# Kernel tuning notes

Measured on AMD Instinct MI355X. Metric: run time of the kernel, lower is better.

Reference implementation:

```python
import jax, jax.numpy as jnp
import numpy as np

STRIDE = 1
PADDING = 1
DILATION = 1


def setup_inputs() -> dict:
    key = jax.random.key(0)
    k1, k2 = jax.random.split(key)
    x = jax.random.normal(k1, (32, 256, 56, 56), dtype=jnp.float32)
    # weight (C_out, C_in, kh, kw); the torch module reformats this to CSR but
    # the computed convolution is mathematically identical to a dense conv.
    W = jax.random.normal(k2, (256, 256, 3, 3), dtype=jnp.float32) * 0.05
    return {"x": x, "W": W}


def reference(x, W):
    # Faithful to SparseConv2D.forward in Inference_Sparse mode: a standard
    # 2D convolution (groups=1, no bias) with stride/padding/dilation.
    out = jax.lax.conv_general_dilated(
        x, W,
        window_strides=(STRIDE, STRIDE),
        padding=[(PADDING, PADDING), (PADDING, PADDING)],
        rhs_dilation=(DILATION, DILATION),
        dimension_numbers=("NCHW", "OIHW", "NCHW"),
    )
    return out
```

## Files before the change

### kernel.cpp

```cpp
#include <hip/hip_runtime.h>

typedef __bf16 bf16_t;
typedef __attribute__((ext_vector_type(8))) __bf16 bf16x8;
typedef __attribute__((ext_vector_type(4))) float f32x4;

#define IMG_H 56
#define IMG_W 56
#define CIN 256
#define COUT 256
#define TH 8
#define TW 16
#define XR 10
#define XCOL 18
#define CK 32
#define PH 58
#define PW 58
#define NPIX (XR * XCOL)
#define NUNIT (NPIX * 5)
#define NISSUE ((NUNIT + 63) / 64)
#define XS_ELEMS (NPIX * 40)

#define NBLK 1792
#define CPX  (NBLK / 8)

#define XBF_BYTES ((size_t)32 * PH * PW * CIN * 2)
#define WT_BYTES  ((size_t)9 * COUT * CIN * 2)

__global__ void wt_permute(const float* __restrict__ W, bf16_t* __restrict__ wt2) {
    int u = blockIdx.x * 256 + threadIdx.x;
    int lane = u & 63;
    int fn   = (u >> 6) & 7;
    int half = (u >> 9) & 1;
    int ch   = (u >> 10) & 7;
    int t    = u >> 13;
    int g = lane >> 4, pc = lane & 15;
    int k  = half * 128 + fn * 16 + pc;
    int cb = ch * 32 + g * 8;
    bf16x8 v;
    #pragma unroll
    for (int j = 0; j < 8; ++j)
        v[j] = (bf16_t)W[(k * CIN + cb + j) * 9 + t];
    *(bf16x8*)(wt2 + (size_t)u * 8) = v;
}

#define LSP 258
__global__ __launch_bounds__(256)
void x_to_bf16(const float* __restrict__ x, bf16_t* __restrict__ xbf) {
    __shared__ bf16_t ls[IMG_W * LSP];
    const int n = blockIdx.y, ph = blockIdx.x;
    bf16_t* drow = xbf + (size_t)(n * PH + ph) * PW * CIN;
    const f32x4 zf = {0.f, 0.f, 0.f, 0.f};
    if (ph == 0 || ph == PH - 1) {
        for (int i = threadIdx.x; i < PW * CIN / 8; i += 256)
            ((f32x4*)drow)[i] = zf;
        return;
    }
    for (int i = threadIdx.x; i < 2 * CIN / 8; i += 256) {
        int side = i >> 5, off = i & 31;
        ((f32x4*)(drow + (side ? (size_t)(PW - 1) * CIN : 0)))[off] = zf;
    }
    const int h = ph - 1;
    const float* src = x + ((size_t)n * CIN * IMG_H + h) * IMG_W;
    for (int e = threadIdx.x; e < CIN * IMG_W; e += 256) {
        int c = e / IMG_W, w = e - c * IMG_W;
        ls[w * LSP + c] = (bf16_t)src[(size_t)c * (IMG_H * IMG_W) + w];
    }
    __syncthreads();
    bf16_t* dst = drow + CIN;
    for (int i = threadIdx.x; i < IMG_W * (CIN / 8); i += 256) {
        int w = i >> 5, cp = (i & 31) * 8;
        bf16x8 v;
        #pragma unroll
        for (int j = 0; j < 8; ++j) v[j] = ls[w * LSP + cp + j];
        *(bf16x8*)(dst + (size_t)w * CIN + cp) = v;
    }
}

__global__ __launch_bounds__(256, 3)
void conv_mfma(const bf16_t* __restrict__ xbf, const bf16_t* __restrict__ wt2,
               float* __restrict__ out) {
    __shared__ __align__(16) bf16_t xs[2][XS_ELEMS];

    const int tid  = threadIdx.x;
    const int lane = tid & 63;
    const int wid  = tid >> 6;

    const int hw      = blockIdx.x;
    const int logical = (hw & 7) * CPX + (hw >> 3);
    const int bk = logical & 1;
    int tmp = logical >> 1;
    const int wx = tmp & 3;  tmp >>= 2;
    const int hy = tmp % 7;
    const int n  = tmp / 7;
    const int h0 = hy * TH;
    const int w0 = wx * TW;

    const int wm   = wid >> 1;
    const int kq2  = wid & 1;
    const int pc   = lane & 15;
    const int g    = lane >> 4;

    f32x4 acc[4][4] = {};
    const bf16_t* wfrag = wt2 + (size_t)lane * 8 + (size_t)bk * 4096
                              + (size_t)kq2 * 2048;
    const bf16_t* xn = xbf + (size_t)n * (PH * PW * CIN);

    int soff[4];
    #pragma unroll
    for (int s = 0; s < 4; ++s) {
        int j = wid + s * 4;
        int u = j * 64 + lane;
        int p = u / 5, q = u - p * 5;
        bool ok = (j < NISSUE) && (u < NUNIT) && (q < 4);
        int r = p / XCOL, col = p - r * XCOL;
        int w = w0 + col; if (w > PW - 1) w = PW - 1;
        int rr = (r > XR - 1) ? (XR - 1) : r;
        soff[s] = ok ? (((h0 + rr) * PW + w) * CIN + q * 8) : -1;
    }

    auto STAGE = [&](int buf, int ch) {
        #pragma unroll
        for (int s = 0; s < 4; ++s)
            if (soff[s] >= 0)
                __builtin_amdgcn_global_load_lds(
                    (const __attribute__((address_space(1))) void*)(xn + soff[s] + ch * CK),
                    (__attribute__((address_space(3))) void*)(&xs[buf][(wid + s * 4) * 512]),
                    16, 0, 0);
    };

    bf16x8 bcur[4], bnext[4];
    #pragma unroll
    for (int q = 0; q < 4; ++q)
        bcur[q] = *(const bf16x8*)(wfrag + q * 512);
    STAGE(0, 0);
    __syncthreads();

    for (int ch = 0; ch < 8; ++ch) {
        const int cur = ch & 1;
        const bf16_t* wch = wfrag + (size_t)ch * 8192;

        #pragma unroll
        for (int dw = 0; dw < 3; ++dw) {
            bf16x8 a[6];
            #pragma unroll
            for (int r = 0; r < 6; ++r)
                a[r] = *(const bf16x8*)&xs[cur][((wm * 4 + r) * XCOL + pc + dw) * 40 + g * 8];
            #pragma unroll
            for (int dh = 0; dh < 3; ++dh) {
                const bool lastTap = (dw == 2) && (dh == 2);
                const bool doPf = !(lastTap && ch == 7);
                if (doPf) {
                    const int tn = (dh < 2) ? ((dh + 1) * 3 + dw) : (dw + 1);
                    const bf16_t* wp = lastTap ? (wch + 8192)
                                               : (wch + (size_t)tn * 65536);
                    #pragma unroll
                    for (int q = 0; q < 4; ++q)
                        bnext[q] = *(const bf16x8*)(wp + q * 512);
                }
                if (dw == 0 && dh == 1 && ch < 7)
                    STAGE(cur ^ 1, ch + 1);
                __builtin_amdgcn_s_setprio(1);
                #pragma unroll
                for (int fm = 0; fm < 4; ++fm)
                    #pragma unroll
                    for (int q = 0; q < 4; ++q)
                        acc[fm][q] = __builtin_amdgcn_mfma_f32_16x16x32_bf16(
                            a[fm + dh], bcur[q], acc[fm][q], 0, 0, 0);
                __builtin_amdgcn_s_setprio(0);
                if (doPf) {
                    #pragma unroll
                    for (int q = 0; q < 4; ++q) bcur[q] = bnext[q];
                }
            }
        }
        __syncthreads();
    }

    const int wcol = w0 + g * 4;
    if (wcol < IMG_W) {
        #pragma unroll
        for (int fm = 0; fm < 4; ++fm) {
            int hh = h0 + wm * 4 + fm;
            #pragma unroll
            for (int q = 0; q < 4; ++q) {
                int k = bk * 128 + kq2 * 64 + q * 16 + pc;
                *(f32x4*)&out[((n * COUT + k) * IMG_H + hh) * IMG_W + wcol] = acc[fm][q];
            }
        }
    }
}

#define CPAD 40
__global__ __launch_bounds__(256, 2)
void conv_mfma_v2(const float* __restrict__ x, const bf16_t* __restrict__ wt2,
                  float* __restrict__ out) {
    __shared__ bf16_t xsl[XR * XCOL * CPAD];
    const int tid  = threadIdx.x;
    const int lane = tid & 63;
    const int wid  = tid >> 6;
    const int n    = blockIdx.z;
    const int h0   = blockIdx.y * TH;
    const int w0   = blockIdx.x * TW;
    const int wm   = wid >> 1;
    const int half = wid & 1;
    const int pc = lane & 15;
    const int g  = lane >> 4;
    const int c0 = g * 8;
    f32x4 acc[4][8] = {};
    const bf16_t* wch_base = wt2 + (size_t)lane * 8 + (size_t)half * 4096;
    for (int ch = 0; ch < 8; ++ch) {
        __syncthreads();
        for (int e = tid; e < XR * XCOL * CK; e += 256) {
            int col = e % XCOL;
            int r   = (e / XCOL) % XR;
            int ci  = e / (XCOL * XR);
            int hh = h0 - 1 + r;
            int ww = w0 - 1 + col;
            float v = 0.f;
            if ((unsigned)hh < (unsigned)IMG_H && (unsigned)ww < (unsigned)IMG_W)
                v = x[((n * CIN + ch * CK + ci) * IMG_H + hh) * IMG_W + ww];
            xsl[(r * XCOL + col) * CPAD + ci] = (bf16_t)v;
        }
        __syncthreads();
        const bf16_t* wch = wch_base + (size_t)ch * 8192;
        #pragma unroll 3
        for (int t = 0; t < 9; ++t) {
            const int dh = t / 3, dw = t % 3;
            const bf16_t* wp = wch + (size_t)t * 65536;
            bf16x8 b[8];
            #pragma unroll
            for (int fn = 0; fn < 8; ++fn)
                b[fn] = *(const bf16x8*)(wp + fn * 512);
            bf16x8 a[4];
            #pragma unroll
            for (int fm = 0; fm < 4; ++fm)
                a[fm] = *(const bf16x8*)&xsl[((wm * 4 + fm + dh) * XCOL + (pc + dw)) * CPAD + c0];
            #pragma unroll
            for (int fm = 0; fm < 4; ++fm)
                #pragma unroll
                for (int fn = 0; fn < 8; ++fn)
                    acc[fm][fn] = __builtin_amdgcn_mfma_f32_16x16x32_bf16(
                        a[fm], b[fn], acc[fm][fn], 0, 0, 0);
        }
    }
    const int wcol = w0 + g * 4;
    if (wcol < IMG_W) {
        #pragma unroll
        for (int fm = 0; fm < 4; ++fm) {
            int hh = h0 + wm * 4 + fm;
            #pragma unroll
            for (int fn = 0; fn < 8; ++fn) {
                int k = half * 128 + fn * 16 + pc;
                *(f32x4*)&out[((n * COUT + k) * IMG_H + hh) * IMG_W + wcol] = acc[fm][fn];
            }
        }
    }
}

__global__ void conv_naive(const float* __restrict__ x, const float* __restrict__ W,
                           float* __restrict__ out, int total) {
    int i = blockIdx.x * 256 + threadIdx.x;
    if (i >= total) return;
    int w = i % IMG_W;
    int h = (i / IMG_W) % IMG_H;
    int k = (i / (IMG_W * IMG_H)) % COUT;
    int n = i / (IMG_W * IMG_H * COUT);
    float s = 0.f;
    for (int c = 0; c < CIN; ++c) {
        #pragma unroll
        for (int dh = 0; dh < 3; ++dh) {
            int hh = h + dh - 1;
            if ((unsigned)hh >= (unsigned)IMG_H) continue;
            #pragma unroll
            for (int dw = 0; dw < 3; ++dw) {
                int ww = w + dw - 1;
                if ((unsigned)ww >= (unsigned)IMG_W) continue;
                s += x[((n * CIN + c) * IMG_H + hh) * IMG_W + ww] *
                     W[((k * CIN + c) * 3 + dh) * 3 + dw];
            }
        }
    }
    out[i] = s;
}

extern "C" void kernel_launch(void* const* d_in, const int* in_sizes, int n_in,
                              void* d_out, int out_size, void* d_ws, size_t ws_size,
                              hipStream_t stream) {
    const float* x = (const float*)d_in[0];
    const float* W = (const float*)d_in[1];
    float* out = (float*)d_out;

    if (ws_size >= XBF_BYTES + WT_BYTES) {
        bf16_t* xbf = (bf16_t*)d_ws;
        bf16_t* wt2 = (bf16_t*)((char*)d_ws + XBF_BYTES);
        wt_permute<<<dim3(288), dim3(256), 0, stream>>>(W, wt2);
        x_to_bf16<<<dim3(PH, 32), dim3(256), 0, stream>>>(x, xbf);
        conv_mfma<<<dim3(NBLK), dim3(256), 0, stream>>>(xbf, wt2, out);
    } else if (ws_size >= WT_BYTES) {
        bf16_t* wt2 = (bf16_t*)d_ws;
        wt_permute<<<dim3(288), dim3(256), 0, stream>>>(W, wt2);
        conv_mfma_v2<<<dim3(4, 7, 32), dim3(256), 0, stream>>>(x, wt2, out);
    } else {
        int total = 32 * COUT * IMG_H * IMG_W;
        conv_naive<<<dim3((total + 255) / 256), dim3(256), 0, stream>>>(x, W, out, total);
    }
}
```

Baseline: 144.7 us.

## Switch main conv kernel from 16x16x32 to 32x32x16 bf16 MFMA tiles

Replaces the 16x16x32 MFMA inner loop with 32x32x16 MFMAs, each covering two output rows by 16 columns against 32 output channels. The weight permutation gets a matching fragment layout, the LDS A-fragment loads are re-indexed, and the epilogue is rewritten for the 32x32 accumulator layout. The old permutation is kept for the fallback v2 kernel. The aim is fewer MFMA issues and fewer register operand reads per FLOP. It changes the LDS read pattern and register pressure, which may cause bank conflicts.

Result: slower. 176.7 us (+22.2%).

```diff
diff --git a/kernel.cpp b/kernel.cpp
--- a/kernel.cpp
+++ b/kernel.cpp
@@ -3,6 +3,7 @@
 typedef __bf16 bf16_t;
 typedef __attribute__((ext_vector_type(8))) __bf16 bf16x8;
 typedef __attribute__((ext_vector_type(4))) float f32x4;
+typedef __attribute__((ext_vector_type(16))) float f32x16;
 
 #define IMG_H 56
 #define IMG_W 56
@@ -29,6 +30,25 @@
 __global__ void wt_permute(const float* __restrict__ W, bf16_t* __restrict__ wt2) {
     int u = blockIdx.x * 256 + threadIdx.x;
     int lane = u & 63;
+    int frag = u >> 6;
+    int ks   = frag & 1;
+    int nf   = (frag >> 1) & 1;
+    int kq2  = (frag >> 2) & 1;
+    int bk   = (frag >> 3) & 1;
+    int ch   = (frag >> 4) & 7;
+    int t    = frag >> 7;
+    int k  = bk * 128 + kq2 * 64 + nf * 32 + (lane & 31);
+    int cb = ch * 32 + ks * 16 + (lane >> 5) * 8;
+    bf16x8 v;
+    #pragma unroll
+    for (int j = 0; j < 8; ++j)
+        v[j] = (bf16_t)W[(k * CIN + cb + j) * 9 + t];
+    *(bf16x8*)(wt2 + (size_t)u * 8) = v;
+}
+
+__global__ void wt_permute16(const float* __restrict__ W, bf16_t* __restrict__ wt2) {
+    int u = blockIdx.x * 256 + threadIdx.x;
+    int lane = u & 63;
     int fn   = (u >> 6) & 7;
     int half = (u >> 9) & 1;
     int ch   = (u >> 10) & 7;
@@ -95,12 +115,13 @@
     const int h0 = hy * TH;
     const int w0 = wx * TW;
 
-    const int wm   = wid >> 1;
-    const int kq2  = wid & 1;
-    const int pc   = lane & 15;
-    const int g    = lane >> 4;
-
-    f32x4 acc[4][4] = {};
+    const int wm    = wid >> 1;
+    const int kq2   = wid & 1;
+    const int pc    = lane & 15;
+    const int prow  = (lane >> 4) & 1;
+    const int chalf = lane >> 5;
+
+    f32x16 acc32[2][2] = {};
     const bf16_t* wfrag = wt2 + (size_t)lane * 8 + (size_t)bk * 4096
                               + (size_t)kq2 * 2048;
     const bf16_t* xn = xbf + (size_t)n * (PH * PW * CIN);
@@ -141,10 +162,14 @@
 
         #pragma unroll
         for (int dw = 0; dw < 3; ++dw) {
-            bf16x8 a[6];
-            #pragma unroll
-            for (int r = 0; r < 6; ++r)
-                a[r] = *(const bf16x8*)&xs[cur][((wm * 4 + r) * XCOL + pc + dw) * 40 + g * 8];
+            bf16x8 a32[5][2];
+            #pragma unroll
+            for (int re = 0; re < 5; ++re)
+                #pragma unroll
+                for (int ks = 0; ks < 2; ++ks)
+                    a32[re][ks] = *(const bf16x8*)&xs[cur][
+                        ((wm * 4 + re + prow) * XCOL + pc + dw) * 40
+                        + ks * 16 + chalf * 8];
             #pragma unroll
             for (int dh = 0; dh < 3; ++dh) {
                 const bool lastTap = (dw == 2) && (dh == 2);
@@ -161,11 +186,14 @@
                     STAGE(cur ^ 1, ch + 1);
                 __builtin_amdgcn_s_setprio(1);
                 #pragma unroll
-                for (int fm = 0; fm < 4; ++fm)
+                for (int ks = 0; ks < 2; ++ks)
                     #pragma unroll
-                    for (int q = 0; q < 4; ++q)
-                        acc[fm][q] = __builtin_amdgcn_mfma_f32_16x16x32_bf16(
-                            a[fm + dh], bcur[q], acc[fm][q], 0, 0, 0);
+                    for (int mf = 0; mf < 2; ++mf)
+                        #pragma unroll
+                        for (int nf = 0; nf < 2; ++nf)
+                            acc32[mf][nf] = __builtin_amdgcn_mfma_f32_32x32x16_bf16(
+                                a32[mf * 2 + dh][ks], bcur[nf * 2 + ks],
+                                acc32[mf][nf], 0, 0, 0);
                 __builtin_amdgcn_s_setprio(0);
                 if (doPf) {
                     #pragma unroll
@@ -176,15 +204,23 @@
         __syncthreads();
     }
 
-    const int wcol = w0 + g * 4;
-    if (wcol < IMG_W) {
-        #pragma unroll
-        for (int fm = 0; fm < 4; ++fm) {
-            int hh = h0 + wm * 4 + fm;
-            #pragma unroll
-            for (int q = 0; q < 4; ++q) {
-                int k = bk * 128 + kq2 * 64 + q * 16 + pc;
-                *(f32x4*)&out[((n * COUT + k) * IMG_H + hh) * IMG_W + wcol] = acc[fm][q];
+    #pragma unroll
+    for (int mf = 0; mf < 2; ++mf) {
+        #pragma unroll
+        for (int nf = 0; nf < 2; ++nf) {
+            const int k = bk * 128 + kq2 * 64 + nf * 32 + (lane & 31);
+            #pragma unroll
+            for (int r4 = 0; r4 < 4; ++r4) {
+                const int hh   = h0 + wm * 4 + mf * 2 + (r4 >> 1);
+                const int wcol = w0 + (r4 & 1) * 8 + 4 * chalf;
+                if (wcol < IMG_W) {
+                    f32x4 v;
+                    v[0] = acc32[mf][nf][r4 * 4 + 0];
+                    v[1] = acc32[mf][nf][r4 * 4 + 1];
+                    v[2] = acc32[mf][nf][r4 * 4 + 2];
+                    v[3] = acc32[mf][nf][r4 * 4 + 3];
+                    *(f32x4*)&out[((n * COUT + k) * IMG_H + hh) * IMG_W + wcol] = v;
+                }
             }
         }
     }
@@ -298,7 +334,7 @@
         conv_mfma<<<dim3(NBLK), dim3(256), 0, stream>>>(xbf, wt2, out);
     } else if (ws_size >= WT_BYTES) {
         bf16_t* wt2 = (bf16_t*)d_ws;
-        wt_permute<<<dim3(288), dim3(256), 0, stream>>>(W, wt2);
+        wt_permute16<<<dim3(288), dim3(256), 0, stream>>>(W, wt2);
         conv_mfma_v2<<<dim3(4, 7, 32), dim3(256), 0, stream>>>(x, wt2, out);
     } else {
         int total = 32 * COUT * IMG_H * IMG_W;
```

## Retile conv_mfma to 8x8 spatial tiles with all 256 output channels per block

Applied to the files above, without the earlier changes.

The main MFMA kernel's spatial tile changes from 8x16 (plus a K-half split across blocks) to 8x8 with each block computing all 256 output channels, four waves each owning 64 channels. The A-fragment mapping now packs two image rows of 8 columns into each 16-row MFMA tile, and the padded-width waste from 56/16 tiling goes away. This removes the duplicate input staging that came from splitting K across two blocks, so each input halo is loaded once per block. In exchange there are fewer blocks (1568), smaller halos with a larger halo-to-interior ratio, more A registers per wave, and a more complex LDS read pattern that may cause bank conflicts.

After: 155.2 us. 1.07x slower.

```diff
diff --git a/kernel.cpp b/kernel.cpp
--- a/kernel.cpp
+++ b/kernel.cpp
@@ -9,18 +9,18 @@
 #define CIN 256
 #define COUT 256
 #define TH 8
-#define TW 16
+#define TW 8
 #define XR 10
-#define XCOL 18
+#define XCOL 10
 #define CK 32
 #define PH 58
 #define PW 58
 #define NPIX (XR * XCOL)
 #define NUNIT (NPIX * 5)
-#define NISSUE ((NUNIT + 63) / 64)
-#define XS_ELEMS (NPIX * 40)
-
-#define NBLK 1792
+#define NISSUE 8
+#define XS_ELEMS 4096
+
+#define NBLK 1568
 #define CPX  (NBLK / 8)
 
 #define XBF_BYTES ((size_t)32 * PH * PW * CIN * 2)
@@ -87,40 +87,37 @@
 
     const int hw      = blockIdx.x;
     const int logical = (hw & 7) * CPX + (hw >> 3);
-    const int bk = logical & 1;
-    int tmp = logical >> 1;
-    const int wx = tmp & 3;  tmp >>= 2;
-    const int hy = tmp % 7;
-    const int n  = tmp / 7;
-    const int h0 = hy * TH;
-    const int w0 = wx * TW;
-
-    const int wm   = wid >> 1;
-    const int kq2  = wid & 1;
+    const int n   = logical / 49;
+    const int rem = logical - n * 49;
+    const int hy  = rem / 7;
+    const int wx  = rem - hy * 7;
+    const int h0  = hy * TH;
+    const int w0  = wx * TW;
+
     const int pc   = lane & 15;
     const int g    = lane >> 4;
+    const int arow = pc >> 3;
+    const int awc  = pc & 7;
 
     f32x4 acc[4][4] = {};
-    const bf16_t* wfrag = wt2 + (size_t)lane * 8 + (size_t)bk * 4096
-                              + (size_t)kq2 * 2048;
+    const bf16_t* wfrag = wt2 + (size_t)lane * 8 + (size_t)(wid >> 1) * 4096
+                              + (size_t)(wid & 1) * 2048;
     const bf16_t* xn = xbf + (size_t)n * (PH * PW * CIN);
 
-    int soff[4];
+    int soff[2];
     #pragma unroll
-    for (int s = 0; s < 4; ++s) {
+    for (int s = 0; s < 2; ++s) {
         int j = wid + s * 4;
         int u = j * 64 + lane;
         int p = u / 5, q = u - p * 5;
-        bool ok = (j < NISSUE) && (u < NUNIT) && (q < 4);
+        bool ok = (u < NUNIT) && (q < 4);
         int r = p / XCOL, col = p - r * XCOL;
-        int w = w0 + col; if (w > PW - 1) w = PW - 1;
-        int rr = (r > XR - 1) ? (XR - 1) : r;
-        soff[s] = ok ? (((h0 + rr) * PW + w) * CIN + q * 8) : -1;
+        soff[s] = ok ? (((h0 + r) * PW + (w0 + col)) * CIN + q * 8) : -1;
     }
 
     auto STAGE = [&](int buf, int ch) {
         #pragma unroll
-        for (int s = 0; s < 4; ++s)
+        for (int s = 0; s < 2; ++s)
             if (soff[s] >= 0)
                 __builtin_amdgcn_global_load_lds(
                     (const __attribute__((address_space(1))) void*)(xn + soff[s] + ch * CK),
@@ -141,10 +138,11 @@
 
         #pragma unroll
         for (int dw = 0; dw < 3; ++dw) {
-            bf16x8 a[6];
-            #pragma unroll
-            for (int r = 0; r < 6; ++r)
-                a[r] = *(const bf16x8*)&xs[cur][((wm * 4 + r) * XCOL + pc + dw) * 40 + g * 8];
+            bf16x8 a[9];
+            #pragma unroll
+            for (int j = 0; j < 9; ++j)
+                a[j] = *(const bf16x8*)&xs[cur][
+                    ((arow + j) * XCOL + awc + dw) * 40 + g * 8];
             #pragma unroll
             for (int dh = 0; dh < 3; ++dh) {
                 const bool lastTap = (dw == 2) && (dh == 2);
@@ -165,7 +163,7 @@
                     #pragma unroll
                     for (int q = 0; q < 4; ++q)
                         acc[fm][q] = __builtin_amdgcn_mfma_f32_16x16x32_bf16(
-                            a[fm + dh], bcur[q], acc[fm][q], 0, 0, 0);
+                            a[fm * 2 + dh], bcur[q], acc[fm][q], 0, 0, 0);
                 __builtin_amdgcn_s_setprio(0);
                 if (doPf) {
                     #pragma unroll
@@ -176,31 +174,32 @@
         __syncthreads();
     }
 
-    const int wcol = w0 + g * 4;
-    if (wcol < IMG_W) {
-        #pragma unroll
-        for (int fm = 0; fm < 4; ++fm) {
-            int hh = h0 + wm * 4 + fm;
-            #pragma unroll
-            for (int q = 0; q < 4; ++q) {
-                int k = bk * 128 + kq2 * 64 + q * 16 + pc;
-                *(f32x4*)&out[((n * COUT + k) * IMG_H + hh) * IMG_W + wcol] = acc[fm][q];
-            }
-        }
-    }
-}
-
+    const int hhb  = h0 + (g >> 1);
+    const int wcol = w0 + (g & 1) * 4;
+    #pragma unroll
+    for (int fm = 0; fm < 4; ++fm) {
+        const int hh = hhb + fm * 2;
+        #pragma unroll
+        for (int q = 0; q < 4; ++q) {
+            const int k = wid * 64 + q * 16 + pc;
+            *(f32x4*)&out[((n * COUT + k) * IMG_H + hh) * IMG_W + wcol] = acc[fm][q];
+        }
+    }
+}
+
+#define FXR 10
+#define FXCOL 18
 #define CPAD 40
 __global__ __launch_bounds__(256, 2)
 void conv_mfma_v2(const float* __restrict__ x, const bf16_t* __restrict__ wt2,
                   float* __restrict__ out) {
-    __shared__ bf16_t xsl[XR * XCOL * CPAD];
+    __shared__ bf16_t xsl[FXR * FXCOL * CPAD];
     const int tid  = threadIdx.x;
     const int lane = tid & 63;
     const int wid  = tid >> 6;
     const int n    = blockIdx.z;
-    const int h0   = blockIdx.y * TH;
-    const int w0   = blockIdx.x * TW;
+    const int h0   = blockIdx.y * 8;
+    const int w0   = blockIdx.x * 16;
     const int wm   = wid >> 1;
     const int half = wid & 1;
     const int pc = lane & 15;
@@ -210,16 +209,16 @@
     const bf16_t* wch_base = wt2 + (size_t)lane * 8 + (size_t)half * 4096;
     for (int ch = 0; ch < 8; ++ch) {
         __syncthreads();
-        for (int e = tid; e < XR * XCOL * CK; e += 256) {
-            int col = e % XCOL;
-            int r   = (e / XCOL) % XR;
-            int ci  = e / (XCOL * XR);
+        for (int e = tid; e < FXR * FXCOL * CK; e += 256) {
+            int col = e % FXCOL;
+            int r   = (e / FXCOL) % FXR;
+            int ci  = e / (FXCOL * FXR);
             int hh = h0 - 1 + r;
             int ww = w0 - 1 + col;
             float v = 0.f;
             if ((unsigned)hh < (unsigned)IMG_H && (unsigned)ww < (unsigned)IMG_W)
                 v = x[((n * CIN + ch * CK + ci) * IMG_H + hh) * IMG_W + ww];
-            xsl[(r * XCOL + col) * CPAD + ci] = (bf16_t)v;
+            xsl[(r * FXCOL + col) * CPAD + ci] = (bf16_t)v;
         }
         __syncthreads();
         const bf16_t* wch = wch_base + (size_t)ch * 8192;
@@ -234,7 +233,7 @@
             bf16x8 a[4];
             #pragma unroll
             for (int fm = 0; fm < 4; ++fm)
-                a[fm] = *(const bf16x8*)&xsl[((wm * 4 + fm + dh) * XCOL + (pc + dw)) * CPAD + c0];
+                a[fm] = *(const bf16x8*)&xsl[((wm * 4 + fm + dh) * FXCOL + (pc + dw)) * CPAD + c0];
             #pragma unroll
             for (int fm = 0; fm < 4; ++fm)
                 #pragma unroll
```
